# Kernel optimization log

Hardware: AMD Instinct MI355X
Metric: run time of the kernel (lower is better)

## Reference

```python
import jax, jax.numpy as jnp
import numpy as np

B, T, C = 4, 2048, 1024
HEAD = 64  # n_embd // n_heads


def setup_inputs() -> dict:
    key = jax.random.key(0)
    kx, kk, kq, kv = jax.random.split(key, 4)
    x = jax.random.normal(kx, (B, T, C), dtype=jnp.float32)
    # nn.Linear(n_embd, head_size, bias=False) weights have shape [head_size, n_embd]
    s = 1.0 / np.sqrt(C)
    Wk = jax.random.normal(kk, (HEAD, C), dtype=jnp.float32) * s
    Wq = jax.random.normal(kq, (HEAD, C), dtype=jnp.float32) * s
    Wv = jax.random.normal(kv, (HEAD, C), dtype=jnp.float32) * s
    return {"x": x, "Wk": Wk, "Wq": Wq, "Wv": Wv}


def reference(x, Wk, Wq, Wv):
    Bx, Tx, Cx = x.shape
    k = jnp.einsum("btc,hc->bth", x, Wk)  # [B,T,HEAD]
    q = jnp.einsum("btc,hc->bth", x, Wq)
    v = jnp.einsum("btc,hc->bth", x, Wv)
    # NOTE: original scales by C**-0.5 (C = n_embd), not head_size**-0.5
    scale = Cx ** (-0.5)
    wei = jnp.einsum("bth,bsh->bts", q, k) * scale  # [B,T,T]
    causal = jnp.tril(jnp.ones((Tx, Tx), dtype=bool))
    wei = jnp.where(causal, wei, -jnp.inf)
    wei = jax.nn.softmax(wei, axis=-1)
    # dropout p=0.0 (eval) -> identity
    out = jnp.einsum("bts,bsh->bth", wei, v)  # [B,T,HEAD]
    return out
```

## Files before the change

### kernel.cpp

```cpp
#include <hip/hip_runtime.h>
#include <math.h>

#define Tn 2048
#define Cn 1024
#define Hn 64

using u16 = unsigned short;
using u32 = unsigned int;
typedef float f32x4 __attribute__((ext_vector_type(4)));
typedef __bf16 bf16x8 __attribute__((ext_vector_type(8)));
typedef u16 u16x8 __attribute__((ext_vector_type(8)));
typedef u32 u32x4 __attribute__((ext_vector_type(4)));

__device__ __forceinline__ u16 f2bf(float f) {
    return __builtin_bit_cast(u16, static_cast<__bf16>(f));
}

__global__ __launch_bounds__(256) void wpack_kernel(
    const float* __restrict__ Wk, const float* __restrict__ Wq,
    const float* __restrict__ Wv, u16* __restrict__ wp)
{
    int slot = blockIdx.x * 256 + threadIdx.x;
    int n16  = slot >> 11;
    int rem  = slot & 2047;
    int kc   = rem >> 6;
    int lane = rem & 63;
    int l15 = lane & 15, lg = lane >> 4;
    int col = n16 * 16 + l15;
    const float* __restrict__ Wm = (col < 64) ? Wk : (col < 128) ? Wq : Wv;
    float sc = (col >= 64 && col < 128) ? 0.03125f : 1.0f;
    const float* src = &Wm[(size_t)(col & 63) * Cn + kc * 32 + lg * 8];
    float4 lo = *reinterpret_cast<const float4*>(src);
    float4 hi = *reinterpret_cast<const float4*>(src + 4);
    u16x8 o;
    o[0] = f2bf(lo.x * sc); o[1] = f2bf(lo.y * sc);
    o[2] = f2bf(lo.z * sc); o[3] = f2bf(lo.w * sc);
    o[4] = f2bf(hi.x * sc); o[5] = f2bf(hi.y * sc);
    o[6] = f2bf(hi.z * sc); o[7] = f2bf(hi.w * sc);
    *reinterpret_cast<u16x8*>(&wp[(size_t)slot * 8]) = o;
}

__global__ __launch_bounds__(256) void qkv_proj(
    const float* __restrict__ x, const u16* __restrict__ wp,
    u16* __restrict__ kb, u16* __restrict__ qb, u16* __restrict__ vb)
{
    __shared__ float xs[2][32 * 68];

    const int tid  = threadIdx.x;
    const int lane = tid & 63;
    const int w    = tid >> 6;
    const int rg   = w & 1;
    const int cg   = w >> 1;
    const int l15  = lane & 15;
    const int lg   = lane >> 4;

    const int row0 = blockIdx.x * 32;
    const int sr   = tid >> 4;
    const int scc  = (tid & 15) << 2;

    f32x4 acc[6];
#pragma unroll
    for (int nt = 0; nt < 6; ++nt)
#pragma unroll
        for (int r = 0; r < 4; ++r) acc[nt][r] = 0.f;

    const float* __restrict__ xsrc0 = &x[(size_t)(row0 + sr) * Cn + scc];
    const float* __restrict__ xsrc1 = &x[(size_t)(row0 + sr + 16) * Cn + scc];
    const u16* __restrict__ wbase = wp + (size_t)cg * 6 * 32 * 64 * 8;

    float4 ga = *reinterpret_cast<const float4*>(xsrc0);
    float4 gb = *reinterpret_cast<const float4*>(xsrc1);
    *reinterpret_cast<float4*>(&xs[0][sr * 68 + scc]) = ga;
    *reinterpret_cast<float4*>(&xs[0][(sr + 16) * 68 + scc]) = gb;
    __syncthreads();

    for (int ks = 0; ks < 16; ++ks) {
        const int cur = ks & 1;
        if (ks < 15) {
            ga = *reinterpret_cast<const float4*>(xsrc0 + (ks + 1) * 64);
            gb = *reinterpret_cast<const float4*>(xsrc1 + (ks + 1) * 64);
        }
#pragma unroll
        for (int kc2 = 0; kc2 < 2; ++kc2) {
            const float* ap = &xs[cur][(rg * 16 + l15) * 68 + kc2 * 32 + (lg << 3)];
            f32x4 a0 = *reinterpret_cast<const f32x4*>(ap);
            f32x4 a1 = *reinterpret_cast<const f32x4*>(ap + 4);
            bf16x8 a;
            a[0] = (__bf16)a0[0]; a[1] = (__bf16)a0[1];
            a[2] = (__bf16)a0[2]; a[3] = (__bf16)a0[3];
            a[4] = (__bf16)a1[0]; a[5] = (__bf16)a1[1];
            a[6] = (__bf16)a1[2]; a[7] = (__bf16)a1[3];
            const int kcg = ks * 2 + kc2;
#pragma unroll
            for (int nt = 0; nt < 6; ++nt) {
                bf16x8 bfr = *reinterpret_cast<const bf16x8*>(
                    &wbase[(size_t)((nt * 32 + kcg) * 64 + lane) * 8]);
                acc[nt] = __builtin_amdgcn_mfma_f32_16x16x32_bf16(a, bfr, acc[nt], 0, 0, 0);
            }
        }
        if (ks < 15) {
            *reinterpret_cast<float4*>(&xs[cur ^ 1][sr * 68 + scc]) = ga;
            *reinterpret_cast<float4*>(&xs[cur ^ 1][(sr + 16) * 68 + scc]) = gb;
        }
        __syncthreads();
    }

#pragma unroll
    for (int nt = 0; nt < 6; ++nt) {
        const int col0 = cg * 96 + nt * 16;
        const int mat  = col0 >> 6;
        u16* __restrict__ ob = (mat == 0) ? kb : (mat == 1) ? qb : vb;
        const int h = (col0 & 63) + l15;
#pragma unroll
        for (int reg = 0; reg < 4; ++reg) {
            const int grow = row0 + rg * 16 + (lg << 2) + reg;
            ob[(size_t)grow * Hn + h] = f2bf(acc[nt][reg]);
        }
    }
}

__global__ __launch_bounds__(256) void attn(
    const u16* __restrict__ qb, const u16* __restrict__ kb,
    const u16* __restrict__ vb, float* __restrict__ Opart,
    float* __restrict__ mlb, float* __restrict__ out)
{
    __shared__ u16 Ks[2][64 * 72];
    __shared__ u16 VTs[2][64 * 72];

    const int tid  = threadIdx.x;
    const int lane = tid & 63;
    const int w    = tid >> 6;
    const int g    = w >> 1;
    const int p    = w & 1;
    const int l15  = lane & 15;
    const int lg   = lane >> 4;

    const int bid = (blockIdx.x & 7) * 80 + (blockIdx.x >> 3);
    const int b = bid / 160;
    const int r = bid % 160;
    int gq = 3;
    while (8 * gq * (gq + 1) > r) --gq;
    const int rr = r - 8 * gq * (gq + 1);
    const int qt = gq * 16 + rr / (gq + 1);
    const int c  = rr % (gq + 1);
    const int c8 = c * 8;

    const int t0  = qt * 32;
    const int wr0 = t0 + g * 16;
    const int nkt = (qt >> 1) + 1;
    const int rounds = (nkt - c8 + 1) >> 1 < 4 ? (nkt - c8 + 1) >> 1 : 4;
    const size_t kvbase = (size_t)b * Tn * Hn;

    bf16x8 qf[2];
    {
        const u16* qrow = qb + ((size_t)(b * Tn + wr0 + l15)) * Hn;
        qf[0] = *reinterpret_cast<const bf16x8*>(&qrow[(lg << 3)]);
        qf[1] = *reinterpret_cast<const bf16x8*>(&qrow[32 + (lg << 3)]);
    }

    f32x4 o[4];
    float m = -INFINITY, ls = 0.f;
#pragma unroll
    for (int nt = 0; nt < 4; ++nt)
#pragma unroll
        for (int rg2 = 0; rg2 < 4; ++rg2) o[nt][rg2] = 0.f;

    const int srcA = l15 + ((lane >> 4) & 1) * 32;
    const int srcB = srcA + 16;
    const bool hiSel = ((lg >> 1) & 1) != 0;

    for (int s = 0; s < rounds; ++s) {
        const int kt0 = c8 + 2 * s, kt1 = kt0 + 1;
        {
#pragma unroll
            for (int i = 0; i < 2; ++i) {
                int cc = tid + 256 * i;
                int rr2 = cc >> 3, cb = (cc & 7) << 3;
                *reinterpret_cast<u16x8*>(&Ks[0][rr2 * 72 + cb]) =
                    *reinterpret_cast<const u16x8*>(&kb[kvbase + (size_t)(kt0 * 64 + rr2) * Hn + cb]);
            }
#pragma unroll
            for (int i = 0; i < 2; ++i) {
                int cc = tid + 256 * i;
                int k = cc & 63, d0 = (cc >> 6) << 3;
                u16x8 v = *reinterpret_cast<const u16x8*>(&vb[kvbase + (size_t)(kt0 * 64 + k) * Hn + d0]);
#pragma unroll
                for (int j = 0; j < 8; ++j) VTs[0][(d0 + j) * 72 + k] = v[j];
            }
        }
        if (kt1 < nkt) {
#pragma unroll
            for (int i = 0; i < 2; ++i) {
                int cc = tid + 256 * i;
                int rr2 = cc >> 3, cb = (cc & 7) << 3;
                *reinterpret_cast<u16x8*>(&Ks[1][rr2 * 72 + cb]) =
                    *reinterpret_cast<const u16x8*>(&kb[kvbase + (size_t)(kt1 * 64 + rr2) * Hn + cb]);
            }
#pragma unroll
            for (int i = 0; i < 2; ++i) {
                int cc = tid + 256 * i;
                int k = cc & 63, d0 = (cc >> 6) << 3;
                u16x8 v = *reinterpret_cast<const u16x8*>(&vb[kvbase + (size_t)(kt1 * 64 + k) * Hn + d0]);
#pragma unroll
                for (int j = 0; j < 8; ++j) VTs[1][(d0 + j) * 72 + k] = v[j];
            }
        }
        __syncthreads();

        const int mykt = kt0 + p;
        if (mykt < nkt) {
            f32x4 sf[4];
#pragma unroll
            for (int nt = 0; nt < 4; ++nt)
#pragma unroll
                for (int rg2 = 0; rg2 < 4; ++rg2) sf[nt][rg2] = 0.f;
#pragma unroll
            for (int kc = 0; kc < 2; ++kc) {
#pragma unroll
                for (int nt = 0; nt < 4; ++nt) {
                    bf16x8 kf = *reinterpret_cast<const bf16x8*>(
                        &Ks[p][(nt * 16 + l15) * 72 + kc * 32 + (lg << 3)]);
                    sf[nt] = __builtin_amdgcn_mfma_f32_16x16x32_bf16(kf, qf[kc], sf[nt], 0, 0, 0);
                }
            }
            if (mykt * 64 + 63 > wr0) {
                const int tq = wr0 + l15;
#pragma unroll
                for (int nt = 0; nt < 4; ++nt) {
#pragma unroll
                    for (int reg = 0; reg < 4; ++reg) {
                        int kg = mykt * 64 + nt * 16 + (lg << 2) + reg;
                        if (kg > tq) sf[nt][reg] = -INFINITY;
                    }
                }
            }
            float tm = sf[0][0];
#pragma unroll
            for (int nt = 0; nt < 4; ++nt)
#pragma unroll
                for (int reg = 0; reg < 4; ++reg) tm = fmaxf(tm, sf[nt][reg]);
            tm = fmaxf(tm, __shfl_xor(tm, 16, 64));
            tm = fmaxf(tm, __shfl_xor(tm, 32, 64));
            if (!__all((tm <= m + 8.f) ? 1 : 0)) {
                float nm = fmaxf(m, tm);
                float al = __expf(m - nm);
                ls *= al;
                float alo[4];
#pragma unroll
                for (int reg = 0; reg < 4; ++reg)
                    alo[reg] = __shfl(al, (lg << 2) | reg, 64);
#pragma unroll
                for (int nt = 0; nt < 4; ++nt)
#pragma unroll
                    for (int reg = 0; reg < 4; ++reg) o[nt][reg] *= alo[reg];
                m = nm;
            }
            float pvv[4][4];
            float rs = 0.f;
#pragma unroll
            for (int nt = 0; nt < 4; ++nt)
#pragma unroll
                for (int reg = 0; reg < 4; ++reg) {
                    pvv[nt][reg] = __expf(sf[nt][reg] - m);
                    rs += pvv[nt][reg];
                }
            rs += __shfl_xor(rs, 16, 64);
            rs += __shfl_xor(rs, 32, 64);
            ls += rs;
            u32 wv[4][2];
#pragma unroll
            for (int nt = 0; nt < 4; ++nt)
#pragma unroll
                for (int h = 0; h < 2; ++h)
                    wv[nt][h] = (u32)f2bf(pvv[nt][2 * h]) |
                                ((u32)f2bf(pvv[nt][2 * h + 1]) << 16);
            bf16x8 pa[2];
#pragma unroll
            for (int kc = 0; kc < 2; ++kc) {
                u32 a0 = __shfl(wv[kc * 2][0], srcA, 64);
                u32 b0 = __shfl(wv[kc * 2 + 1][0], srcA, 64);
                u32 a1 = __shfl(wv[kc * 2][1], srcA, 64);
                u32 b1 = __shfl(wv[kc * 2 + 1][1], srcA, 64);
                u32 a2 = __shfl(wv[kc * 2][0], srcB, 64);
                u32 b2 = __shfl(wv[kc * 2 + 1][0], srcB, 64);
                u32 a3 = __shfl(wv[kc * 2][1], srcB, 64);
                u32 b3 = __shfl(wv[kc * 2 + 1][1], srcB, 64);
                u32x4 pw;
                pw[0] = hiSel ? b0 : a0;
                pw[1] = hiSel ? b1 : a1;
                pw[2] = hiSel ? b2 : a2;
                pw[3] = hiSel ? b3 : a3;
                pa[kc] = __builtin_bit_cast(bf16x8, pw);
            }
#pragma unroll
            for (int kc = 0; kc < 2; ++kc) {
#pragma unroll
                for (int nt = 0; nt < 4; ++nt) {
                    bf16x8 vf = *reinterpret_cast<const bf16x8*>(
                        &VTs[p][(nt * 16 + l15) * 72 + kc * 32 + (lg << 3)]);
                    o[nt] = __builtin_amdgcn_mfma_f32_16x16x32_bf16(pa[kc], vf, o[nt], 0, 0, 0);
                }
            }
        }
        __syncthreads();
    }

    float* slab = reinterpret_cast<float*>(&Ks[0][0]);
    float* sb = slab + g * (24 * 64);
    if (p == 1) {
#pragma unroll
        for (int nt = 0; nt < 4; ++nt)
#pragma unroll
            for (int reg = 0; reg < 4; ++reg)
                sb[(nt * 4 + reg) * 64 + lane] = o[nt][reg];
        if (lane < 16) {
            sb[1024 + lane] = m;
            sb[1040 + lane] = ls;
        }
    }
    __syncthreads();
    if (p == 0) {
        float mA[4], lA[4], mB[4], lB[4];
#pragma unroll
        for (int reg = 0; reg < 4; ++reg) {
            int q = (lg << 2) | reg;
            mA[reg] = __shfl(m, q, 64);
            lA[reg] = __shfl(ls, q, 64);
            mB[reg] = sb[1024 + q];
            lB[reg] = sb[1040 + q];
        }
        if (gq == 0) {
#pragma unroll
            for (int reg = 0; reg < 4; ++reg) {
                float ms = fmaxf(mA[reg], mB[reg]);
                float aA = __expf(mA[reg] - ms);
                float aB = __expf(mB[reg] - ms);
                float inv = 1.0f / (aA * lA[reg] + aB * lB[reg]);
                int grow = t0 + g * 16 + (lg << 2) + reg;
                float* orow = out + ((size_t)(b * Tn) + grow) * Hn;
#pragma unroll
                for (int nt = 0; nt < 4; ++nt)
                    orow[nt * 16 + l15] =
                        (aA * o[nt][reg] + aB * sb[(nt * 4 + reg) * 64 + lane]) * inv;
            }
        } else {
            const size_t pidx = (size_t)(b * 64 + qt) * 4 + c;
            float* __restrict__ ob = Opart + pidx * 2048;
#pragma unroll
            for (int reg = 0; reg < 4; ++reg) {
                float ms = fmaxf(mA[reg], mB[reg]);
                float aA = __expf(mA[reg] - ms);
                float aB = __expf(mB[reg] - ms);
                int row32 = g * 16 + (lg << 2) + reg;
                if (l15 == 0) {
                    float* mlp = mlb + pidx * 64 + row32 * 2;
                    mlp[0] = ms;
                    mlp[1] = aA * lA[reg] + aB * lB[reg];
                }
#pragma unroll
                for (int nt = 0; nt < 4; ++nt)
                    ob[row32 * 64 + nt * 16 + l15] =
                        aA * o[nt][reg] + aB * sb[(nt * 4 + reg) * 64 + lane];
            }
        }
    }
}

__global__ __launch_bounds__(256) void attn_merge(
    const float* __restrict__ Opart, const float* __restrict__ mlb,
    float* __restrict__ out)
{
    const int bid = blockIdx.x;
    const int b  = bid / 48;
    const int qt = 16 + bid % 48;
    const int nch = (qt >> 4) + 1;
    const int t = threadIdx.x;
    const int row = t >> 3, d0 = (t & 7) << 3;
    const size_t pbase = (size_t)(b * 64 + qt) * 4;

    float mc[4], lc[4];
#pragma unroll
    for (int cc = 0; cc < 4; ++cc) {
        if (cc < nch) {
            const float* mlp = mlb + (pbase + cc) * 64 + row * 2;
            mc[cc] = mlp[0];
            lc[cc] = mlp[1];
        } else { mc[cc] = -INFINITY; lc[cc] = 0.f; }
    }
    float mfin = fmaxf(fmaxf(mc[0], mc[1]), fmaxf(mc[2], mc[3]));

    float wgt[4], l = 0.f;
#pragma unroll
    for (int cc = 0; cc < 4; ++cc) {
        wgt[cc] = (cc < nch) ? __expf(mc[cc] - mfin) : 0.f;
        l += lc[cc] * wgt[cc];
    }

    f32x4 O0 = {0.f, 0.f, 0.f, 0.f}, O1 = {0.f, 0.f, 0.f, 0.f};
#pragma unroll
    for (int cc = 0; cc < 4; ++cc) {
        if (cc < nch) {
            const float* op = Opart + (pbase + cc) * 2048 + row * 64 + d0;
            f32x4 c0 = *reinterpret_cast<const f32x4*>(op);
            f32x4 c1 = *reinterpret_cast<const f32x4*>(op + 4);
            O0 += c0 * wgt[cc];
            O1 += c1 * wgt[cc];
        }
    }
    float inv = 1.f / l;
    float* orow = out + ((size_t)(b * Tn + qt * 32 + row)) * Hn + d0;
    *reinterpret_cast<f32x4*>(orow)     = O0 * inv;
    *reinterpret_cast<f32x4*>(orow + 4) = O1 * inv;
}

extern "C" void kernel_launch(void* const* d_in, const int* in_sizes, int n_in,
                              void* d_out, int out_size, void* d_ws, size_t ws_size,
                              hipStream_t stream) {
    const float* x  = (const float*)d_in[0];
    const float* Wk = (const float*)d_in[1];
    const float* Wq = (const float*)d_in[2];
    const float* Wv = (const float*)d_in[3];
    float* out = (float*)d_out;

    const size_t rows = (size_t)4 * Tn;
    u16* kbuf = (u16*)d_ws;
    u16* qbuf = kbuf + rows * Hn;
    u16* vbuf = qbuf + rows * Hn;
    u16* wpk  = vbuf + rows * Hn;
    float* Opart = (float*)(wpk + 196608);
    float* mlb   = Opart + (size_t)256 * 4 * 2048;

    wpack_kernel<<<96, 256, 0, stream>>>(Wk, Wq, Wv, wpk);
    qkv_proj<<<256, 256, 0, stream>>>(x, wpk, kbuf, qbuf, vbuf);
    attn<<<640, 256, 0, stream>>>(qbuf, kbuf, vbuf, Opart, mlb, out);
    attn_merge<<<192, 256, 0, stream>>>(Opart, mlb, out);
}
```

Before: 42.38 us.

## Prefetch next K/V round into registers and double-buffer shared tiles

After: 45.04 us. 1.06x slower.

```diff
diff --git a/kernel.cpp b/kernel.cpp
--- a/kernel.cpp
+++ b/kernel.cpp
@@ -124,8 +124,8 @@
     const u16* __restrict__ vb, float* __restrict__ Opart,
     float* __restrict__ mlb, float* __restrict__ out)
 {
-    __shared__ u16 Ks[2][64 * 72];
-    __shared__ u16 VTs[2][64 * 72];
+    __shared__ u16 Ks[4][64 * 72];
+    __shared__ u16 VTs[4][64 * 72];
 
     const int tid  = threadIdx.x;
     const int lane = tid & 63;
@@ -151,6 +151,10 @@
     const int rounds = (nkt - c8 + 1) >> 1 < 4 ? (nkt - c8 + 1) >> 1 : 4;
     const size_t kvbase = (size_t)b * Tn * Hn;
 
+    const int krow0 = tid >> 3,          kcb0 = (tid & 7) << 3;
+    const int krow1 = (tid + 256) >> 3,  kcb1 = ((tid + 256) & 7) << 3;
+    const int vk0 = tid & 63,  vd0 = (tid >> 6) << 3;
+
     bf16x8 qf[2];
     {
         const u16* qrow = qb + ((size_t)(b * Tn + wr0 + l15)) * Hn;
@@ -158,6 +162,52 @@
         qf[1] = *reinterpret_cast<const bf16x8*>(&qrow[32 + (lg << 3)]);
     }
 
+    u16x8 krg[2][2], vrg[2][2];
+#define LOADR(s)                                                              \
+    {                                                                         \
+        const int kt0_ = c8 + 2 * (s), kt1_ = kt0_ + 1;                       \
+        krg[0][0] = *reinterpret_cast<const u16x8*>(                          \
+            &kb[kvbase + (size_t)(kt0_ * 64 + krow0) * Hn + kcb0]);           \
+        krg[0][1] = *reinterpret_cast<const u16x8*>(                          \
+            &kb[kvbase + (size_t)(kt0_ * 64 + krow1) * Hn + kcb1]);           \
+        vrg[0][0] = *reinterpret_cast<const u16x8*>(                          \
+            &vb[kvbase + (size_t)(kt0_ * 64 + vk0) * Hn + vd0]);              \
+        vrg[0][1] = *reinterpret_cast<const u16x8*>(                          \
+            &vb[kvbase + (size_t)(kt0_ * 64 + vk0) * Hn + vd0 + 32]);         \
+        if (kt1_ < nkt) {                                                     \
+            krg[1][0] = *reinterpret_cast<const u16x8*>(                      \
+                &kb[kvbase + (size_t)(kt1_ * 64 + krow0) * Hn + kcb0]);       \
+            krg[1][1] = *reinterpret_cast<const u16x8*>(                      \
+                &kb[kvbase + (size_t)(kt1_ * 64 + krow1) * Hn + kcb1]);       \
+            vrg[1][0] = *reinterpret_cast<const u16x8*>(                      \
+                &vb[kvbase + (size_t)(kt1_ * 64 + vk0) * Hn + vd0]);          \
+            vrg[1][1] = *reinterpret_cast<const u16x8*>(                      \
+                &vb[kvbase + (size_t)(kt1_ * 64 + vk0) * Hn + vd0 + 32]);     \
+        }                                                                     \
+    }
+
+#define WRITER(s)                                                             \
+    {                                                                         \
+        const int bs_ = 2 * ((s) & 1);                                        \
+        const int kt1_ = c8 + 2 * (s) + 1;                                    \
+        *reinterpret_cast<u16x8*>(&Ks[bs_][krow0 * 72 + kcb0]) = krg[0][0];   \
+        *reinterpret_cast<u16x8*>(&Ks[bs_][krow1 * 72 + kcb1]) = krg[0][1];   \
+        _Pragma("unroll")                                                     \
+        for (int j = 0; j < 8; ++j) {                                         \
+            VTs[bs_][(vd0 + j) * 72 + vk0]      = vrg[0][0][j];               \
+            VTs[bs_][(vd0 + 32 + j) * 72 + vk0] = vrg[0][1][j];               \
+        }                                                                     \
+        if (kt1_ < nkt) {                                                     \
+            *reinterpret_cast<u16x8*>(&Ks[bs_ + 1][krow0 * 72 + kcb0]) = krg[1][0]; \
+            *reinterpret_cast<u16x8*>(&Ks[bs_ + 1][krow1 * 72 + kcb1]) = krg[1][1]; \
+            _Pragma("unroll")                                                 \
+            for (int j = 0; j < 8; ++j) {                                     \
+                VTs[bs_ + 1][(vd0 + j) * 72 + vk0]      = vrg[1][0][j];       \
+                VTs[bs_ + 1][(vd0 + 32 + j) * 72 + vk0] = vrg[1][1][j];       \
+            }                                                                 \
+        }                                                                     \
+    }
+
     f32x4 o[4];
     float m = -INFINITY, ls = 0.f;
 #pragma unroll
@@ -169,45 +219,16 @@
     const int srcB = srcA + 16;
     const bool hiSel = ((lg >> 1) & 1) != 0;
 
+    LOADR(0);
+    WRITER(0);
+    __syncthreads();
+
     for (int s = 0; s < rounds; ++s) {
-        const int kt0 = c8 + 2 * s, kt1 = kt0 + 1;
-        {
-#pragma unroll
-            for (int i = 0; i < 2; ++i) {
-                int cc = tid + 256 * i;
-                int rr2 = cc >> 3, cb = (cc & 7) << 3;
-                *reinterpret_cast<u16x8*>(&Ks[0][rr2 * 72 + cb]) =
-                    *reinterpret_cast<const u16x8*>(&kb[kvbase + (size_t)(kt0 * 64 + rr2) * Hn + cb]);
-            }
-#pragma unroll
-            for (int i = 0; i < 2; ++i) {
-                int cc = tid + 256 * i;
-                int k = cc & 63, d0 = (cc >> 6) << 3;
-                u16x8 v = *reinterpret_cast<const u16x8*>(&vb[kvbase + (size_t)(kt0 * 64 + k) * Hn + d0]);
-#pragma unroll
-                for (int j = 0; j < 8; ++j) VTs[0][(d0 + j) * 72 + k] = v[j];
-            }
-        }
-        if (kt1 < nkt) {
-#pragma unroll
-            for (int i = 0; i < 2; ++i) {
-                int cc = tid + 256 * i;
-                int rr2 = cc >> 3, cb = (cc & 7) << 3;
-                *reinterpret_cast<u16x8*>(&Ks[1][rr2 * 72 + cb]) =
-                    *reinterpret_cast<const u16x8*>(&kb[kvbase + (size_t)(kt1 * 64 + rr2) * Hn + cb]);
-            }
-#pragma unroll
-            for (int i = 0; i < 2; ++i) {
-                int cc = tid + 256 * i;
-                int k = cc & 63, d0 = (cc >> 6) << 3;
-                u16x8 v = *reinterpret_cast<const u16x8*>(&vb[kvbase + (size_t)(kt1 * 64 + k) * Hn + d0]);
-#pragma unroll
-                for (int j = 0; j < 8; ++j) VTs[1][(d0 + j) * 72 + k] = v[j];
-            }
-        }
-        __syncthreads();
-
-        const int mykt = kt0 + p;
+        const bool pre = (s + 1 < rounds);
+        if (pre) LOADR(s + 1);
+
+        const int bs = 2 * (s & 1);
+        const int mykt = c8 + 2 * s + p;
         if (mykt < nkt) {
             f32x4 sf[4];
 #pragma unroll
@@ -219,7 +240,7 @@
 #pragma unroll
                 for (int nt = 0; nt < 4; ++nt) {
                     bf16x8 kf = *reinterpret_cast<const bf16x8*>(
-                        &Ks[p][(nt * 16 + l15) * 72 + kc * 32 + (lg << 3)]);
+                        &Ks[bs + p][(nt * 16 + l15) * 72 + kc * 32 + (lg << 3)]);
                     sf[nt] = __builtin_amdgcn_mfma_f32_16x16x32_bf16(kf, qf[kc], sf[nt], 0, 0, 0);
                 }
             }
@@ -297,11 +318,12 @@
 #pragma unroll
                 for (int nt = 0; nt < 4; ++nt) {
                     bf16x8 vf = *reinterpret_cast<const bf16x8*>(
-                        &VTs[p][(nt * 16 + l15) * 72 + kc * 32 + (lg << 3)]);
+                        &VTs[bs + p][(nt * 16 + l15) * 72 + kc * 32 + (lg << 3)]);
                     o[nt] = __builtin_amdgcn_mfma_f32_16x16x32_bf16(pa[kc], vf, o[nt], 0, 0, 0);
                 }
             }
         }
+        if (pre) WRITER(s + 1);
         __syncthreads();
     }
 
@@ -364,6 +386,8 @@
             }
         }
     }
+#undef LOADR
+#undef WRITER
 }
 
 __global__ __launch_bounds__(256) void attn_merge(
```
